# Performance work log

Hardware: AMD Instinct MI355X
Metric: run time of the kernel (lower is better)

The kernel has to match this reference:

```python
import jax, jax.numpy as jnp
import numpy as np

E, H, G, NB, T_OBS, A, PRED = 64, 128, 8, 32.0, 8, 512, 12


def setup_inputs() -> dict:
    key = jax.random.key(0)
    ks = jax.random.split(key, 12)
    s = lambda fan: 1.0 / np.sqrt(fan)
    obs = jax.random.uniform(ks[0], (T_OBS, A, 2), dtype=jnp.float32, minval=-40.0, maxval=40.0)
    mask = jax.random.uniform(ks[1], (A,)) > 0.1
    W_e = jax.random.normal(ks[2], (E, 2), jnp.float32) * s(2)
    b_e = jnp.zeros((E,), jnp.float32)
    W_p = jax.random.normal(ks[3], (H, G * G * H), jnp.float32) * s(G * G * H)
    b_p = jnp.zeros((H,), jnp.float32)
    W_ih = jax.random.normal(ks[4], (4 * H, E + H), jnp.float32) * s(E + H)
    W_hh = jax.random.normal(ks[5], (4 * H, H), jnp.float32) * s(H)
    b_ih = jnp.zeros((4 * H,), jnp.float32)
    b_hh = jnp.zeros((4 * H,), jnp.float32)
    W_o = jax.random.normal(ks[6], (5, H), jnp.float32) * s(H)
    b_o = jnp.zeros((5,), jnp.float32)
    return dict(obs=obs, mask=mask, W_e=W_e, b_e=b_e, W_p=W_p, b_p=b_p,
                W_ih=W_ih, W_hh=W_hh, b_ih=b_ih, b_hh=b_hh, W_o=W_o, b_o=b_o)


def _social_pool(hidden, pos, mask, W_p, b_p):
    # hidden (A,H), pos (A,2), mask (A,) -> pooled (A,H)
    a, h = hidden.shape
    cell = 2.0 * NB / G
    vi = mask & jnp.all(~jnp.isnan(pos), axis=-1)           # valid agents
    rel = pos[None, :, :] - pos[:, None, :]                  # rel[i,j] = pos[j]-pos[i]
    rx, ry = rel[..., 0], rel[..., 1]
    inb = (jnp.abs(rx) < NB) & (jnp.abs(ry) < NB)
    col = jnp.clip(jnp.floor((rx + NB) / cell).astype(jnp.int32), 0, G - 1)
    row = jnp.clip(jnp.floor((ry + NB) / cell).astype(jnp.int32), 0, G - 1)
    cell_id = row * G + col                                  # (A,A)
    eye = jnp.eye(a, dtype=bool)
    valid = vi[:, None] & vi[None, :] & (~eye) & inb
    onehot = jax.nn.one_hot(cell_id, G * G, dtype=hidden.dtype) * valid[..., None].astype(hidden.dtype)
    grid = jnp.einsum('ijg,jh->igh', onehot, hidden)         # (A, G*G, H) scatter-sum
    pooled = grid.reshape(a, G * G * h) @ W_p.T + b_p
    return jnp.where(vi[:, None], pooled, 0.0)


def _lstm(inp, h, c, W_ih, W_hh, b_ih, b_hh):
    z = inp @ W_ih.T + h @ W_hh.T + b_ih + b_hh
    i, f, g, o = jnp.split(z, 4, axis=-1)
    i, f, o = jax.nn.sigmoid(i), jax.nn.sigmoid(f), jax.nn.sigmoid(o)
    g = jnp.tanh(g)
    c = f * c + i * g
    return o * jnp.tanh(c), c


def _forward(obs, mask, W_e, b_e, W_p, b_p, W_ih, W_hh, b_ih, b_hh, W_o, b_o):
    a = obs.shape[1]
    obs_clean = jnp.where(jnp.isnan(obs), 0.0, obs)
    h0 = jnp.zeros((a, H), obs.dtype)
    c0 = jnp.zeros((a, H), obs.dtype)

    def enc_step(carry, pos):
        h, c = carry
        emb = jax.nn.relu(pos @ W_e.T + b_e)
        soc = _social_pool(h, pos, mask, W_p, b_p)
        h, c = _lstm(jnp.concatenate([emb, soc], -1), h, c, W_ih, W_hh, b_ih, b_hh)
        return (h, c), None

    (h, c), _ = jax.lax.scan(enc_step, (h0, c0), obs_clean)

    cur0 = jnp.where(mask[:, None], obs_clean[-1], 0.0)

    def dec_step(carry, _):
        h, c, cur = carry
        emb = jax.nn.relu(cur @ W_e.T + b_e)
        soc = _social_pool(h, cur, mask, W_p, b_p)
        h, c = _lstm(jnp.concatenate([emb, soc], -1), h, c, W_ih, W_hh, b_ih, b_hh)
        raw = h @ W_o.T + b_o                                # (A,5)
        mu = raw[:, :2]
        sg = jnp.exp(raw[:, 2:4]) + 1e-6
        rh = jnp.tanh(raw[:, 4])
        cur = cur + mu * mask[:, None].astype(raw.dtype)
        return (h, c, cur), (cur, sg, rh)

    _, (pred_mu, pred_sigma, pred_rho) = jax.lax.scan(dec_step, (h, c, cur0), None, length=PRED)
    return pred_mu, pred_sigma, pred_rho


def reference(obs, mask, W_e, b_e, W_p, b_p, W_ih, W_hh, b_ih, b_hh, W_o, b_o):
    return _forward(obs, mask, W_e, b_e, W_p, b_p, W_ih, W_hh, b_ih, b_hh, W_o, b_o)
```

## Files before the change

kernel.cpp:

```cpp
#include <hip/hip_runtime.h>

#define T_OBS 8
#define PRED  12

typedef __attribute__((ext_vector_type(8))) short bf16x8;
typedef __attribute__((ext_vector_type(4))) float f32x4;
typedef __attribute__((ext_vector_type(2))) unsigned long long u64x2;
#define MFMA16(a,b,c) __builtin_amdgcn_mfma_f32_16x16x32_bf16((a),(b),(c),0,0,0)

#define WP_OFF    0
#define WZ_OFF    2097152
#define BZ_OFF    2424832
#define MASK_OFF  2426880
#define CUR_OFF   2428928
#define HG_OFF    2433024
#define CST_OFF   2564096
#define XIN_OFF   2826240
#define U_OFF     3022848
#define LSTP_OFF  11411456
#define NVP_OFF   16130048

static __device__ __forceinline__ unsigned short f2bf(float x){
    union { float f; unsigned u; } v; v.f = x;
    unsigned r = v.u + 0x7fffu + ((v.u >> 16) & 1u);
    return (unsigned short)(r >> 16);
}
static __device__ __forceinline__ unsigned pack2(float a, float b){
    return (unsigned)f2bf(a) | ((unsigned)f2bf(b) << 16);
}
static __device__ __forceinline__ float bf2lo(unsigned v){ return __uint_as_float(v << 16); }
static __device__ __forceinline__ float bf2hi(unsigned v){ return __uint_as_float(v & 0xffff0000u); }
static __device__ __forceinline__ float sigm_f(float x){ return 1.f / (1.f + __expf(-x)); }
static __device__ __forceinline__ float tanh_f(float x){
    float e = __expf(-2.f * fabsf(x));
    float t = (1.f - e) / (1.f + e);
    return copysignf(t, x);
}

__global__ __launch_bounds__(256) void prep(
    const float* __restrict__ obs, const float* __restrict__ Wp,
    const float* __restrict__ Wih, const float* __restrict__ Whh,
    const float* __restrict__ bih, const float* __restrict__ bhh,
    const unsigned char* __restrict__ mraw,
    unsigned short* __restrict__ wp_bf, unsigned short* __restrict__ wz,
    float* __restrict__ bz, int* __restrict__ mski,
    unsigned* __restrict__ hg32, float* __restrict__ cst,
    short* __restrict__ lst_pre, int* __restrict__ nv_pre)
{
    __shared__ int maskl[512];
    __shared__ float2 posl[512];
    __shared__ short  celll[512];
    __shared__ int mflagA, mflagB;
    const int bid = blockIdx.x, tid = threadIdx.x;
    const int i0 = bid * 256 + tid, stride = 512 * 256;

    if (tid == 0){ mflagA = 0; mflagB = 0; }
    __syncthreads();
    for (int j = tid; j < 512; j += 256){
        unsigned char b = mraw[j];
        if (b && (j & 3))        atomicAdd(&mflagA, 1);
        if (b && ((j & 7) == 4)) atomicAdd(&mflagB, 1);
    }
    __syncthreads();
    for (int j = tid; j < 512; j += 256){
        int v;
        if (mflagA)      v = mraw[j] ? 1 : 0;
        else if (mflagB) v = ((const int*)mraw)[j] ? 1 : 0;
        else             v = ((const long long*)mraw)[j] ? 1 : 0;
        maskl[j] = v;
        if (bid == 0) mski[j] = v;
    }
    __syncthreads();

    for (int i = i0; i < 524288; i += stride)
        ((unsigned*)wp_bf)[i] = pack2(Wp[2*i], Wp[2*i + 1]);
    for (int i = i0; i < 81920; i += stride){
        int n = (2*i) / 320, k = (2*i) - n*320;
        float w0 = (k < 192)     ? Wih[n*192 + k]     : Whh[n*128 + k - 192];
        float w1 = (k + 1 < 192) ? Wih[n*192 + k + 1] : Whh[n*128 + k + 1 - 192];
        ((unsigned*)wz)[i] = pack2(w0, w1);
    }
    for (int i = i0; i < 512; i += stride) bz[i] = bih[i] + bhh[i];
    for (int i = i0; i < 32768; i += stride) hg32[i] = 0u;
    for (int i = i0; i < 65536; i += stride) cst[i] = 0.f;

    const int vi = maskl[bid];
    for (int tt = 0; tt <= 8; ++tt){
        const int to = (tt < 8) ? tt : 7;
        __syncthreads();
        for (int j = tid; j < 512; j += 256){
            float px = obs[to*1024 + 2*j], py = obs[to*1024 + 2*j + 1];
            if (isnan(px)) px = 0.f;
            if (isnan(py)) py = 0.f;
            if (tt == 8 && !maskl[j]){ px = 0.f; py = 0.f; }
            posl[j] = make_float2(px, py);
        }
        __syncthreads();
        const float2 pi = posl[bid];
        for (int j = tid; j < 512; j += 256){
            int cc = -1;
            if (vi && j != bid && maskl[j]){
                float rx = posl[j].x - pi.x, ry = posl[j].y - pi.y;
                if (fabsf(rx) < 32.f && fabsf(ry) < 32.f){
                    int col = (int)floorf((rx + 32.f) * 0.125f);
                    int row = (int)floorf((ry + 32.f) * 0.125f);
                    col = min(max(col, 0), 7); row = min(max(row, 0), 7);
                    cc = row*8 + col;
                }
            }
            celll[j] = (short)cc;
        }
        __syncthreads();
        if (tid < 64){
            short* lp = lst_pre + ((long long)tt*512 + bid)*512;
            int base = 0;
            for (int b = 0; b < 8; ++b){
                short cj = celll[b*64 + tid];
                bool val = cj >= 0;
                unsigned long long bal = __ballot(val);
                int pre = __popcll(bal & ((1ull << tid) - 1ull));
                if (val) lp[base + pre] = (short)((b*64 + tid) | ((int)cj << 9));
                base += __popcll(bal);
            }
            if (tid == 0) nv_pre[tt*512 + bid] = base;
        }
    }
}

__global__ __launch_bounds__(256) void ku(
    const unsigned short* __restrict__ hg,
    const unsigned short* __restrict__ wp_bf,
    const float* __restrict__ obs, const float* __restrict__ W_o,
    const float* __restrict__ b_o, const int* __restrict__ mski,
    float* __restrict__ cur, float* __restrict__ out,
    unsigned short* __restrict__ U, int t)
{
    __shared__ unsigned short ustage[32][256];
    const int bid = blockIdx.x, tid = threadIdx.x;

    if (t > T_OBS && tid < 64){
        const int dec_t = t - T_OBS - 1;
        unsigned v = ((const unsigned*)hg)[bid*64 + tid];
        float h0 = bf2lo(v), h1 = bf2hi(v);
        float p[5];
        #pragma unroll
        for (int o = 0; o < 5; ++o)
            p[o] = W_o[o*128 + 2*tid]*h0 + W_o[o*128 + 2*tid + 1]*h1;
        #pragma unroll
        for (int s = 32; s; s >>= 1)
            #pragma unroll
            for (int o = 0; o < 5; ++o) p[o] += __shfl_xor(p[o], s, 64);
        if (tid == 0){
            float mu0 = p[0] + b_o[0], mu1 = p[1] + b_o[1];
            float s0 = __expf(p[2] + b_o[2]) + 1e-6f;
            float s1 = __expf(p[3] + b_o[3]) + 1e-6f;
            float rh = tanh_f(p[4] + b_o[4]);
            float cx, cy;
            if (dec_t == 0){
                cx = obs[7*1024 + bid*2]; cy = obs[7*1024 + bid*2 + 1];
                if (isnan(cx)) cx = 0.f;
                if (isnan(cy)) cy = 0.f;
                if (!mski[bid]){ cx = 0.f; cy = 0.f; }
            } else {
                cx = cur[bid*2]; cy = cur[bid*2 + 1];
            }
            if (mski[bid]){ cx += mu0; cy += mu1; }
            cur[bid*2] = cx; cur[bid*2 + 1] = cy;
            out[dec_t*1024 + bid*2]             = cx;
            out[dec_t*1024 + bid*2 + 1]         = cy;
            out[12288 + dec_t*1024 + bid*2]     = s0;
            out[12288 + dec_t*1024 + bid*2 + 1] = s1;
            out[24576 + dec_t*512 + bid]        = rh;
        }
    }
    if (t >= T_OBS + PRED) return;

    const int mq = bid >> 5, cp = bid & 31;
    const int r0 = mq * 32;
    const int w = tid >> 6, lane = tid & 63;
    const int msub = w & 1, nq = w >> 1;
    const int lrow = lane & 15, lk = (lane >> 4) * 8;
    f32x4 acc[2][4] = {};
    #pragma unroll
    for (int ks = 0; ks < 4; ++ks){
        bf16x8 a = *(const bf16x8*)(hg + (r0 + msub*16 + lrow)*128 + ks*32 + lk);
        #pragma unroll
        for (int cell = 0; cell < 2; ++cell){
            #pragma unroll
            for (int ntl = 0; ntl < 4; ++ntl){
                const unsigned short* bp = wp_bf +
                    ((nq*4 + ntl)*16 + lrow)*8192 + (2*cp + cell)*128 + ks*32 + lk;
                acc[cell][ntl] = MFMA16(a, *(const bf16x8*)bp, acc[cell][ntl]);
            }
        }
    }
    const int crow = (lane >> 4) * 4, ccol = lane & 15;
    #pragma unroll
    for (int cell = 0; cell < 2; ++cell)
        #pragma unroll
        for (int ntl = 0; ntl < 4; ++ntl)
            #pragma unroll
            for (int r = 0; r < 4; ++r)
                ustage[msub*16 + crow + r][cell*128 + (nq*4 + ntl)*16 + ccol]
                    = f2bf(acc[cell][ntl][r]);
    __syncthreads();
    for (int e = tid; e < 1024; e += 256){
        int r = e >> 5, o = e & 31;
        u64x2 v = *(const u64x2*)&ustage[r][o*8];
        __builtin_nontemporal_store(v,
            (u64x2*)((char*)U + ((long long)(r0 + r)*64 + 2*cp)*256 + o*16));
    }
}

__global__ __launch_bounds__(256) void kg(
    const float* __restrict__ obs, const int* __restrict__ mski,
    const unsigned short* __restrict__ U,
    const float* __restrict__ W_e, const float* __restrict__ b_e,
    const float* __restrict__ b_p, const float* __restrict__ cur,
    const short* __restrict__ lst_pre, const int* __restrict__ nv_pre,
    unsigned short* __restrict__ xin, int t)
{
    __shared__ float2 pos[512];
    __shared__ short  cells_s[512];
    __shared__ short  lst[512];
    __shared__ int    nvS;
    __shared__ float  socp[8][128];
    const int bid = blockIdx.x, tid = threadIdx.x;

    float2 pi;
    int n;
    const int vi = mski[bid];

    if (t <= 8){
        const int to = (t < 8) ? t : 7;
        float px = obs[to*1024 + 2*bid], py = obs[to*1024 + 2*bid + 1];
        if (isnan(px)) px = 0.f;
        if (isnan(py)) py = 0.f;
        if (t == 8 && !vi){ px = 0.f; py = 0.f; }
        pi = make_float2(px, py);
        const short* lp = lst_pre + ((long long)t*512 + bid)*512;
        for (int e = tid; e < 512; e += 256) lst[e] = lp[e];
        n = (t == 0) ? 0 : nv_pre[t*512 + bid];
        __syncthreads();
    } else {
        for (int s = 0; s < 2; ++s){
            int j = tid + s*256;
            pos[j] = ((const float2*)cur)[j];
        }
        __syncthreads();
        pi = pos[bid];
        for (int s = 0; s < 2; ++s){
            int j = tid + s*256;
            int cc = -1;
            if (vi && j != bid && mski[j]){
                float rx = pos[j].x - pi.x, ry = pos[j].y - pi.y;
                if (fabsf(rx) < 32.f && fabsf(ry) < 32.f){
                    int col = (int)floorf((rx + 32.f) * 0.125f);
                    int row = (int)floorf((ry + 32.f) * 0.125f);
                    col = min(max(col, 0), 7); row = min(max(row, 0), 7);
                    cc = row*8 + col;
                }
            }
            cells_s[j] = (short)cc;
        }
        __syncthreads();
        if (tid < 64){
            int base = 0;
            for (int b = 0; b < 8; ++b){
                short cj = cells_s[b*64 + tid];
                bool val = cj >= 0;
                unsigned long long bal = __ballot(val);
                int pre = __popcll(bal & ((1ull << tid) - 1ull));
                if (val) lst[base + pre] = (short)((b*64 + tid) | ((int)cj << 9));
                base += __popcll(bal);
            }
            if (tid == 0) nvS = base;
        }
        __syncthreads();
        n = nvS;
    }

    {
        const int slot = tid >> 5, lq = tid & 31;
        const unsigned long long* ub = (const unsigned long long*)U;
        float s0 = 0.f, s1 = 0.f, s2 = 0.f, s3 = 0.f;
        int b4 = 0;
        for (; b4 + 128 <= n; b4 += 128){
            unsigned long long v[16];
            #pragma unroll
            for (int u = 0; u < 16; ++u){
                int pk = lst[b4 + u*8 + slot];
                v[u] = __builtin_nontemporal_load(
                           ub + (pk & 511)*2048 + (pk >> 9)*32 + lq);
            }
            #pragma unroll
            for (int u = 0; u < 16; ++u){
                unsigned lo = (unsigned)v[u], hi = (unsigned)(v[u] >> 32);
                s0 += bf2lo(lo); s1 += bf2hi(lo);
                s2 += bf2lo(hi); s3 += bf2hi(hi);
            }
        }
        for (; b4 + 32 <= n; b4 += 32){
            unsigned long long v[4];
            #pragma unroll
            for (int u = 0; u < 4; ++u){
                int pk = lst[b4 + u*8 + slot];
                v[u] = __builtin_nontemporal_load(
                           ub + (pk & 511)*2048 + (pk >> 9)*32 + lq);
            }
            #pragma unroll
            for (int u = 0; u < 4; ++u){
                unsigned lo = (unsigned)v[u], hi = (unsigned)(v[u] >> 32);
                s0 += bf2lo(lo); s1 += bf2hi(lo);
                s2 += bf2lo(hi); s3 += bf2hi(hi);
            }
        }
        for (; b4 + 8 <= n; b4 += 8){
            int pk = lst[b4 + slot];
            unsigned long long v = __builtin_nontemporal_load(
                                       ub + (pk & 511)*2048 + (pk >> 9)*32 + lq);
            unsigned lo = (unsigned)v, hi = (unsigned)(v >> 32);
            s0 += bf2lo(lo); s1 += bf2hi(lo); s2 += bf2lo(hi); s3 += bf2hi(hi);
        }
        if (b4 + slot < n){
            int pk = lst[b4 + slot];
            unsigned long long v = __builtin_nontemporal_load(
                                       ub + (pk & 511)*2048 + (pk >> 9)*32 + lq);
            unsigned lo = (unsigned)v, hi = (unsigned)(v >> 32);
            s0 += bf2lo(lo); s1 += bf2hi(lo); s2 += bf2lo(hi); s3 += bf2hi(hi);
        }
        f32x4 sv = {s0, s1, s2, s3};
        *(f32x4*)&socp[slot][lq*4] = sv;
    }
    __syncthreads();
    if (tid < 128){
        float s = b_p[tid];
        #pragma unroll
        for (int p = 0; p < 8; ++p) s += socp[p][tid];
        if (!vi) s = 0.f;
        xin[bid*192 + 64 + tid] = f2bf(s);
    } else if (tid < 192){
        int u = tid - 128;
        float e = W_e[u*2]*pi.x + W_e[u*2 + 1]*pi.y + b_e[u];
        xin[bid*192 + u] = f2bf(fmaxf(e, 0.f));
    }
}

__global__ __launch_bounds__(256) void kl(
    const unsigned short* __restrict__ xin, const unsigned short* __restrict__ hg_rd,
    const unsigned short* __restrict__ wz, const float* __restrict__ bz,
    float* __restrict__ cst, unsigned* __restrict__ hg_wr)
{
    __shared__ float zpart[2][4][16][16];
    __shared__ float hst[16][17];
    const int bid = blockIdx.x, tid = threadIdx.x;
    const int rt = bid >> 3, uo = bid & 7;
    const int r0 = rt * 16, u0 = uo * 16;
    const int w = tid >> 6, lane = tid & 63;
    const int gh = w & 1, p = w >> 1;
    const int lrow = lane & 15, lk = (lane >> 4) * 8;

    f32x4 acc[2] = {};
    #pragma unroll
    for (int kk = 0; kk < 5; ++kk){
        const int ks = p*5 + kk;
        const int row = r0 + lrow;
        bf16x8 a;
        if (ks < 6) a = *(const bf16x8*)(xin + row*192 + ks*32 + lk);
        else        a = *(const bf16x8*)(hg_rd + row*128 + (ks - 6)*32 + lk);
        #pragma unroll
        for (int gi = 0; gi < 2; ++gi){
            const int g = gh*2 + gi;
            bf16x8 b = *(const bf16x8*)(wz + (g*128 + u0 + lrow)*320 + ks*32 + lk);
            acc[gi] = MFMA16(a, b, acc[gi]);
        }
    }
    const int crow = (lane >> 4) * 4, ccol = lane & 15;
    #pragma unroll
    for (int gi = 0; gi < 2; ++gi)
        #pragma unroll
        for (int r = 0; r < 4; ++r)
            zpart[p][gh*2 + gi][crow + r][ccol] = acc[gi][r];
    __syncthreads();

    if (tid < 256){
        int row = tid >> 4, lu = tid & 15;
        int unit = u0 + lu;
        float zi = zpart[0][0][row][lu] + zpart[1][0][row][lu] + bz[      unit];
        float zf = zpart[0][1][row][lu] + zpart[1][1][row][lu] + bz[128 + unit];
        float zg = zpart[0][2][row][lu] + zpart[1][2][row][lu] + bz[256 + unit];
        float zo = zpart[0][3][row][lu] + zpart[1][3][row][lu] + bz[384 + unit];
        float ig = sigm_f(zi), fg = sigm_f(zf);
        float gv = tanh_f(zg), og = sigm_f(zo);
        int gi2 = (r0 + row)*128 + unit;
        float cn = fg * cst[gi2] + ig * gv;
        float hn = og * tanh_f(cn);
        cst[gi2] = cn;
        hst[row][lu] = hn;
    }
    __syncthreads();
    if (tid < 128){
        int row = tid >> 3, pp = tid & 7;
        hg_wr[(r0 + row)*64 + uo*8 + pp] = pack2(hst[row][2*pp], hst[row][2*pp + 1]);
    }
}

extern "C" void kernel_launch(void* const* d_in, const int* in_sizes, int n_in,
                              void* d_out, int out_size, void* d_ws, size_t ws_size,
                              hipStream_t stream)
{
    const float* obs  = (const float*)d_in[0];
    const unsigned char* mraw = (const unsigned char*)d_in[1];
    const float* W_e  = (const float*)d_in[2];
    const float* b_e  = (const float*)d_in[3];
    const float* W_p  = (const float*)d_in[4];
    const float* b_p  = (const float*)d_in[5];
    const float* W_ih = (const float*)d_in[6];
    const float* W_hh = (const float*)d_in[7];
    const float* b_ih = (const float*)d_in[8];
    const float* b_hh = (const float*)d_in[9];
    const float* W_o  = (const float*)d_in[10];
    const float* b_o  = (const float*)d_in[11];
    float* out = (float*)d_out;

    char* ws = (char*)d_ws;
    unsigned short* wp_bf = (unsigned short*)(ws + WP_OFF);
    unsigned short* wz_bf = (unsigned short*)(ws + WZ_OFF);
    float* bz   = (float*)(ws + BZ_OFF);
    int*   mski = (int*)  (ws + MASK_OFF);
    float* cur  = (float*)(ws + CUR_OFF);
    unsigned short* hg = (unsigned short*)(ws + HG_OFF);
    float* cst  = (float*)(ws + CST_OFF);
    unsigned short* xin = (unsigned short*)(ws + XIN_OFF);
    unsigned short* U   = (unsigned short*)(ws + U_OFF);
    short* lst_pre = (short*)(ws + LSTP_OFF);
    int*   nv_pre  = (int*)  (ws + NVP_OFF);

    prep<<<512, 256, 0, stream>>>(obs, W_p, W_ih, W_hh, b_ih, b_hh, mraw,
                                  wp_bf, wz_bf, bz, mski, (unsigned*)hg, cst,
                                  lst_pre, nv_pre);

    for (int t = 0; t < T_OBS + PRED; ++t){
        if (t > 0)
            ku<<<512, 256, 0, stream>>>(hg, wp_bf, obs, W_o, b_o, mski,
                                        cur, out, U, t);
        kg<<<512, 256, 0, stream>>>(obs, mski, U, W_e, b_e, b_p, cur,
                                    lst_pre, nv_pre, xin, t);
        kl<<<256, 256, 0, stream>>>(xin, hg, wz_bf, bz, cst, (unsigned*)hg);
    }
    ku<<<512, 256, 0, stream>>>(hg, wp_bf, obs, W_o, b_o, mski,
                                cur, out, U, T_OBS + PRED);
}
```

Before: 533.0 us.

## Fuse per-step pooling, LSTM and projection kernels with device-wide barriers

Replaces the three kernels launched per time step (ku, kg, kl) with a single step kernel. Inside it, a hand-rolled atomic grid barrier separates the gather, LSTM and projection/output phases, and the hidden state is double-buffered so reads and writes do not conflict across steps. This cuts about 60 launches and their gaps down to 20, and moves the decoder output head after the projection within the same step. In exchange it depends on all 512 blocks being co-resident (launch bounds of 2 blocks per CU) for the spin barrier to work. The spin loop has a bailout cap and uses relaxed atomics, which could cause hangs or incorrect results if that assumption fails.

Result: slower. 824.2 us (+54.6%).

```diff
diff --git a/kernel.cpp b/kernel.cpp
--- a/kernel.cpp
+++ b/kernel.cpp
@@ -2,23 +2,42 @@
 
 #define T_OBS 8
 #define PRED  12
+#define NSTEP 20
 
 typedef __attribute__((ext_vector_type(8))) short bf16x8;
 typedef __attribute__((ext_vector_type(4))) float f32x4;
 typedef __attribute__((ext_vector_type(2))) unsigned long long u64x2;
 #define MFMA16(a,b,c) __builtin_amdgcn_mfma_f32_16x16x32_bf16((a),(b),(c),0,0,0)
+#define AS __ATOMIC_RELAXED, __HIP_MEMORY_SCOPE_AGENT
 
 #define WP_OFF    0
 #define WZ_OFF    2097152
 #define BZ_OFF    2424832
 #define MASK_OFF  2426880
 #define CUR_OFF   2428928
-#define HG_OFF    2433024
-#define CST_OFF   2564096
-#define XIN_OFF   2826240
-#define U_OFF     3022848
-#define LSTP_OFF  11411456
-#define NVP_OFF   16130048
+#define HG0_OFF   2433024
+#define HG1_OFF   2564096
+#define CST_OFF   2695168
+#define XIN_OFF   2957312
+#define U_OFF     3153920
+#define LSTP_OFF  11542528
+#define NVP_OFF   16261120
+#define BAR_OFF   16279552
+
+static __device__ __forceinline__ void st32c(void* p, unsigned v){
+    __hip_atomic_store((unsigned*)p, v, AS);
+}
+static __device__ __forceinline__ unsigned ld32c(const void* p){
+    return __hip_atomic_load((const unsigned*)p, AS);
+}
+static __device__ __forceinline__ unsigned long long ld64c(const void* p){
+    return __hip_atomic_load((const unsigned long long*)p, AS);
+}
+static __device__ __forceinline__ bf16x8 ldfragc(const unsigned short* p){
+    union { unsigned long long q[2]; bf16x8 v; } u;
+    u.q[0] = ld64c(p); u.q[1] = ld64c(p + 4);
+    return u.v;
+}
 
 static __device__ __forceinline__ unsigned short f2bf(float x){
     union { float f; unsigned u; } v; v.f = x;
@@ -37,6 +56,25 @@
     return copysignf(t, x);
 }
 
+static __device__ __forceinline__ void gridbar(int* bar, int bid, int target){
+    __syncthreads();
+    if (threadIdx.x == 0){
+        int p = __hip_atomic_fetch_add(&bar[32 + (bid >> 3)*16], 1, AS);
+        if ((p & 7) == 7){
+            int q = __hip_atomic_fetch_add(&bar[16], 1, AS);
+            if ((q & 63) == 63)
+                __hip_atomic_store(&bar[0], target, AS);
+        }
+        int spins = 0;
+        while (__hip_atomic_load(&bar[0], AS) < target){
+            __builtin_amdgcn_s_sleep(1);
+            if (++spins > (1 << 22)) break;
+        }
+        asm volatile("" ::: "memory");
+    }
+    __syncthreads();
+}
+
 __global__ __launch_bounds__(256) void prep(
     const float* __restrict__ obs, const float* __restrict__ Wp,
     const float* __restrict__ Wih, const float* __restrict__ Whh,
@@ -44,8 +82,9 @@
     const unsigned char* __restrict__ mraw,
     unsigned short* __restrict__ wp_bf, unsigned short* __restrict__ wz,
     float* __restrict__ bz, int* __restrict__ mski,
-    unsigned* __restrict__ hg32, float* __restrict__ cst,
-    short* __restrict__ lst_pre, int* __restrict__ nv_pre)
+    unsigned* __restrict__ hg1, float* __restrict__ cst,
+    short* __restrict__ lst_pre, int* __restrict__ nv_pre,
+    int* __restrict__ bar)
 {
     __shared__ int maskl[512];
     __shared__ float2 posl[512];
@@ -81,8 +120,9 @@
         ((unsigned*)wz)[i] = pack2(w0, w1);
     }
     for (int i = i0; i < 512; i += stride) bz[i] = bih[i] + bhh[i];
-    for (int i = i0; i < 32768; i += stride) hg32[i] = 0u;
+    for (int i = i0; i < 32768; i += stride) hg1[i] = 0u;
     for (int i = i0; i < 65536; i += stride) cst[i] = 0.f;
+    for (int i = i0; i < 2048; i += stride) bar[i] = 0;
 
     const int vi = maskl[bid];
     for (int tt = 0; tt <= 8; ++tt){
@@ -127,281 +167,281 @@
     }
 }
 
-__global__ __launch_bounds__(256) void ku(
-    const unsigned short* __restrict__ hg,
-    const unsigned short* __restrict__ wp_bf,
-    const float* __restrict__ obs, const float* __restrict__ W_o,
-    const float* __restrict__ b_o, const int* __restrict__ mski,
-    float* __restrict__ cur, float* __restrict__ out,
-    unsigned short* __restrict__ U, int t)
+union StepSmem {
+    struct { float2 pos[512]; short cells[512]; short lst[512];
+             float socp[8][128]; } a;
+    struct { float zpart[2][4][16][16]; float hst[16][17]; } b;
+    struct { unsigned short ustage[32][256]; } c;
+};
+
+__global__ __launch_bounds__(256, 2) void step(
+    const float* __restrict__ obs, const int* __restrict__ mski,
+    const unsigned short* __restrict__ wp, const unsigned short* __restrict__ wz,
+    const float* __restrict__ bz, const float* __restrict__ b_p,
+    const float* __restrict__ W_e, const float* __restrict__ b_e,
+    const float* __restrict__ W_o, const float* __restrict__ b_o,
+    const short* __restrict__ lst_pre, const int* __restrict__ nv_pre,
+    float* __restrict__ cur, const unsigned short* __restrict__ hg_rd,
+    unsigned short* __restrict__ hg_wr, float* __restrict__ cst,
+    unsigned short* __restrict__ xin, unsigned short* __restrict__ U,
+    int* __restrict__ bar, float* __restrict__ out, int t)
 {
-    __shared__ unsigned short ustage[32][256];
+    __shared__ StepSmem sm;
+    __shared__ int nvS;
     const int bid = blockIdx.x, tid = threadIdx.x;
-
-    if (t > T_OBS && tid < 64){
-        const int dec_t = t - T_OBS - 1;
-        unsigned v = ((const unsigned*)hg)[bid*64 + tid];
-        float h0 = bf2lo(v), h1 = bf2hi(v);
-        float p[5];
+    const int w = tid >> 6, lane = tid & 63;
+    const int lrow = lane & 15, lk = (lane >> 4) * 8;
+    const int crow = (lane >> 4) * 4, ccol = lane & 15;
+
+    {
+        float2 pi;
+        int n;
+        const int vi = mski[bid];
+        if (t <= 8){
+            const int to = (t < 8) ? t : 7;
+            float px = obs[to*1024 + 2*bid], py = obs[to*1024 + 2*bid + 1];
+            if (isnan(px)) px = 0.f;
+            if (isnan(py)) py = 0.f;
+            if (t == 8 && !vi){ px = 0.f; py = 0.f; }
+            pi = make_float2(px, py);
+            const short* lp = lst_pre + ((long long)t*512 + bid)*512;
+            for (int e = tid; e < 512; e += 256) sm.a.lst[e] = lp[e];
+            n = (t == 0) ? 0 : nv_pre[t*512 + bid];
+            __syncthreads();
+        } else {
+            for (int s = 0; s < 2; ++s){
+                int j = tid + s*256;
+                sm.a.pos[j] = ((const float2*)cur)[j];
+            }
+            __syncthreads();
+            pi = sm.a.pos[bid];
+            for (int s = 0; s < 2; ++s){
+                int j = tid + s*256;
+                int cc = -1;
+                if (vi && j != bid && mski[j]){
+                    float rx = sm.a.pos[j].x - pi.x, ry = sm.a.pos[j].y - pi.y;
+                    if (fabsf(rx) < 32.f && fabsf(ry) < 32.f){
+                        int col = (int)floorf((rx + 32.f) * 0.125f);
+                        int row = (int)floorf((ry + 32.f) * 0.125f);
+                        col = min(max(col, 0), 7); row = min(max(row, 0), 7);
+                        cc = row*8 + col;
+                    }
+                }
+                sm.a.cells[j] = (short)cc;
+            }
+            __syncthreads();
+            if (tid < 64){
+                int base = 0;
+                for (int b = 0; b < 8; ++b){
+                    short cj = sm.a.cells[b*64 + tid];
+                    bool val = cj >= 0;
+                    unsigned long long bal = __ballot(val);
+                    int pre = __popcll(bal & ((1ull << tid) - 1ull));
+                    if (val) sm.a.lst[base + pre] = (short)((b*64 + tid) | ((int)cj << 9));
+                    base += __popcll(bal);
+                }
+                if (tid == 0) nvS = base;
+            }
+            __syncthreads();
+            n = nvS;
+        }
+        {
+            const int slot = tid >> 5, lq = tid & 31;
+            const unsigned long long* ub = (const unsigned long long*)U;
+            float s0 = 0.f, s1 = 0.f, s2 = 0.f, s3 = 0.f;
+            int b4 = 0;
+            for (; b4 + 128 <= n; b4 += 128){
+                unsigned long long v[16];
+                #pragma unroll
+                for (int u = 0; u < 16; ++u){
+                    int pk = sm.a.lst[b4 + u*8 + slot];
+                    v[u] = __builtin_nontemporal_load(
+                               ub + (pk & 511)*2048 + (pk >> 9)*32 + lq);
+                }
+                #pragma unroll
+                for (int u = 0; u < 16; ++u){
+                    unsigned lo = (unsigned)v[u], hi = (unsigned)(v[u] >> 32);
+                    s0 += bf2lo(lo); s1 += bf2hi(lo);
+                    s2 += bf2lo(hi); s3 += bf2hi(hi);
+                }
+            }
+            for (; b4 + 32 <= n; b4 += 32){
+                unsigned long long v[4];
+                #pragma unroll
+                for (int u = 0; u < 4; ++u){
+                    int pk = sm.a.lst[b4 + u*8 + slot];
+                    v[u] = __builtin_nontemporal_load(
+                               ub + (pk & 511)*2048 + (pk >> 9)*32 + lq);
+                }
+                #pragma unroll
+                for (int u = 0; u < 4; ++u){
+                    unsigned lo = (unsigned)v[u], hi = (unsigned)(v[u] >> 32);
+                    s0 += bf2lo(lo); s1 += bf2hi(lo);
+                    s2 += bf2lo(hi); s3 += bf2hi(hi);
+                }
+            }
+            for (; b4 + 8 <= n; b4 += 8){
+                int pk = sm.a.lst[b4 + slot];
+                unsigned long long v = __builtin_nontemporal_load(
+                                           ub + (pk & 511)*2048 + (pk >> 9)*32 + lq);
+                unsigned lo = (unsigned)v, hi = (unsigned)(v >> 32);
+                s0 += bf2lo(lo); s1 += bf2hi(lo); s2 += bf2lo(hi); s3 += bf2hi(hi);
+            }
+            if (b4 + slot < n){
+                int pk = sm.a.lst[b4 + slot];
+                unsigned long long v = __builtin_nontemporal_load(
+                                           ub + (pk & 511)*2048 + (pk >> 9)*32 + lq);
+                unsigned lo = (unsigned)v, hi = (unsigned)(v >> 32);
+                s0 += bf2lo(lo); s1 += bf2hi(lo); s2 += bf2lo(hi); s3 += bf2hi(hi);
+            }
+            f32x4 sv = {s0, s1, s2, s3};
+            *(f32x4*)&sm.a.socp[slot][lq*4] = sv;
+        }
+        __syncthreads();
+        unsigned* xin32 = (unsigned*)xin;
+        if (tid < 64){
+            float s0 = b_p[2*tid], s1 = b_p[2*tid + 1];
+            #pragma unroll
+            for (int p = 0; p < 8; ++p){
+                s0 += sm.a.socp[p][2*tid];
+                s1 += sm.a.socp[p][2*tid + 1];
+            }
+            if (!vi){ s0 = 0.f; s1 = 0.f; }
+            st32c(xin32 + bid*96 + 32 + tid, pack2(s0, s1));
+        } else if (tid < 96){
+            int u = tid - 64;
+            float e0 = fmaxf(W_e[(2*u    )*2]*pi.x + W_e[(2*u    )*2 + 1]*pi.y + b_e[2*u    ], 0.f);
+            float e1 = fmaxf(W_e[(2*u + 1)*2]*pi.x + W_e[(2*u + 1)*2 + 1]*pi.y + b_e[2*u + 1], 0.f);
+            st32c(xin32 + bid*96 + u, pack2(e0, e1));
+        }
+    }
+    gridbar(bar, bid, 2*t + 1);
+
+    if (bid < 256){
+        const int rt = bid >> 3, uo = bid & 7;
+        const int r0 = rt * 16, u0 = uo * 16;
+        const int gh = w & 1, p = w >> 1;
+
+        f32x4 acc[2] = {};
         #pragma unroll
-        for (int o = 0; o < 5; ++o)
-            p[o] = W_o[o*128 + 2*tid]*h0 + W_o[o*128 + 2*tid + 1]*h1;
+        for (int kk = 0; kk < 5; ++kk){
+            const int ks = p*5 + kk;
+            const int row = r0 + lrow;
+            bf16x8 a;
+            if (ks < 6) a = ldfragc(xin + row*192 + ks*32 + lk);
+            else        a = *(const bf16x8*)(hg_rd + row*128 + (ks - 6)*32 + lk);
+            #pragma unroll
+            for (int gi = 0; gi < 2; ++gi){
+                const int g = gh*2 + gi;
+                bf16x8 b = *(const bf16x8*)(wz + (g*128 + u0 + lrow)*320 + ks*32 + lk);
+                acc[gi] = MFMA16(a, b, acc[gi]);
+            }
+        }
         #pragma unroll
-        for (int s = 32; s; s >>= 1)
-            #pragma unroll
-            for (int o = 0; o < 5; ++o) p[o] += __shfl_xor(p[o], s, 64);
-        if (tid == 0){
-            float mu0 = p[0] + b_o[0], mu1 = p[1] + b_o[1];
-            float s0 = __expf(p[2] + b_o[2]) + 1e-6f;
-            float s1 = __expf(p[3] + b_o[3]) + 1e-6f;
-            float rh = tanh_f(p[4] + b_o[4]);
-            float cx, cy;
-            if (dec_t == 0){
-                cx = obs[7*1024 + bid*2]; cy = obs[7*1024 + bid*2 + 1];
-                if (isnan(cx)) cx = 0.f;
-                if (isnan(cy)) cy = 0.f;
-                if (!mski[bid]){ cx = 0.f; cy = 0.f; }
-            } else {
-                cx = cur[bid*2]; cy = cur[bid*2 + 1];
-            }
-            if (mski[bid]){ cx += mu0; cy += mu1; }
-            cur[bid*2] = cx; cur[bid*2 + 1] = cy;
-            out[dec_t*1024 + bid*2]             = cx;
-            out[dec_t*1024 + bid*2 + 1]         = cy;
-            out[12288 + dec_t*1024 + bid*2]     = s0;
-            out[12288 + dec_t*1024 + bid*2 + 1] = s1;
-            out[24576 + dec_t*512 + bid]        = rh;
-        }
-    }
-    if (t >= T_OBS + PRED) return;
+        for (int gi = 0; gi < 2; ++gi)
+            #pragma unroll
+            for (int r = 0; r < 4; ++r)
+                sm.b.zpart[p][gh*2 + gi][crow + r][ccol] = acc[gi][r];
+        __syncthreads();
+
+        {
+            int row = tid >> 4, lu = tid & 15;
+            int unit = u0 + lu;
+            float zi = sm.b.zpart[0][0][row][lu] + sm.b.zpart[1][0][row][lu] + bz[      unit];
+            float zf = sm.b.zpart[0][1][row][lu] + sm.b.zpart[1][1][row][lu] + bz[128 + unit];
+            float zg = sm.b.zpart[0][2][row][lu] + sm.b.zpart[1][2][row][lu] + bz[256 + unit];
+            float zo = sm.b.zpart[0][3][row][lu] + sm.b.zpart[1][3][row][lu] + bz[384 + unit];
+            float ig = sigm_f(zi), fg = sigm_f(zf);
+            float gv = tanh_f(zg), og = sigm_f(zo);
+            int gi2 = (r0 + row)*128 + unit;
+            float cn = fg * cst[gi2] + ig * gv;
+            float hn = og * tanh_f(cn);
+            cst[gi2] = cn;
+            sm.b.hst[row][lu] = hn;
+        }
+        __syncthreads();
+        if (tid < 128){
+            int row = tid >> 3, pp = tid & 7;
+            st32c((unsigned*)hg_wr + (r0 + row)*64 + uo*8 + pp,
+                  pack2(sm.b.hst[row][2*pp], sm.b.hst[row][2*pp + 1]));
+        }
+    }
+    gridbar(bar, bid, 2*t + 2);
 
     const int mq = bid >> 5, cp = bid & 31;
-    const int r0 = mq * 32;
-    const int w = tid >> 6, lane = tid & 63;
-    const int msub = w & 1, nq = w >> 1;
-    const int lrow = lane & 15, lk = (lane >> 4) * 8;
-    f32x4 acc[2][4] = {};
-    #pragma unroll
-    for (int ks = 0; ks < 4; ++ks){
-        bf16x8 a = *(const bf16x8*)(hg + (r0 + msub*16 + lrow)*128 + ks*32 + lk);
+    const int r0c = mq * 32;
+    if (t < NSTEP - 1){
+        const int msub = w & 1, nq = w >> 1;
+        bf16x8 afr[4];
         #pragma unroll
-        for (int cell = 0; cell < 2; ++cell){
-            #pragma unroll
-            for (int ntl = 0; ntl < 4; ++ntl){
-                const unsigned short* bp = wp_bf +
-                    ((nq*4 + ntl)*16 + lrow)*8192 + (2*cp + cell)*128 + ks*32 + lk;
-                acc[cell][ntl] = MFMA16(a, *(const bf16x8*)bp, acc[cell][ntl]);
-            }
-        }
-    }
-    const int crow = (lane >> 4) * 4, ccol = lane & 15;
-    #pragma unroll
-    for (int cell = 0; cell < 2; ++cell)
+        for (int ks = 0; ks < 4; ++ks)
+            afr[ks] = ldfragc(hg_wr + (r0c + msub*16 + lrow)*128 + ks*32 + lk);
+        f32x4 acc[2][4] = {};
         #pragma unroll
-        for (int ntl = 0; ntl < 4; ++ntl)
-            #pragma unroll
-            for (int r = 0; r < 4; ++r)
-                ustage[msub*16 + crow + r][cell*128 + (nq*4 + ntl)*16 + ccol]
-                    = f2bf(acc[cell][ntl][r]);
-    __syncthreads();
-    for (int e = tid; e < 1024; e += 256){
-        int r = e >> 5, o = e & 31;
-        u64x2 v = *(const u64x2*)&ustage[r][o*8];
-        __builtin_nontemporal_store(v,
-            (u64x2*)((char*)U + ((long long)(r0 + r)*64 + 2*cp)*256 + o*16));
-    }
-}
-
-__global__ __launch_bounds__(256) void kg(
-    const float* __restrict__ obs, const int* __restrict__ mski,
-    const unsigned short* __restrict__ U,
-    const float* __restrict__ W_e, const float* __restrict__ b_e,
-    const float* __restrict__ b_p, const float* __restrict__ cur,
-    const short* __restrict__ lst_pre, const int* __restrict__ nv_pre,
-    unsigned short* __restrict__ xin, int t)
-{
-    __shared__ float2 pos[512];
-    __shared__ short  cells_s[512];
-    __shared__ short  lst[512];
-    __shared__ int    nvS;
-    __shared__ float  socp[8][128];
-    const int bid = blockIdx.x, tid = threadIdx.x;
-
-    float2 pi;
-    int n;
-    const int vi = mski[bid];
-
-    if (t <= 8){
-        const int to = (t < 8) ? t : 7;
-        float px = obs[to*1024 + 2*bid], py = obs[to*1024 + 2*bid + 1];
-        if (isnan(px)) px = 0.f;
-        if (isnan(py)) py = 0.f;
-        if (t == 8 && !vi){ px = 0.f; py = 0.f; }
-        pi = make_float2(px, py);
-        const short* lp = lst_pre + ((long long)t*512 + bid)*512;
-        for (int e = tid; e < 512; e += 256) lst[e] = lp[e];
-        n = (t == 0) ? 0 : nv_pre[t*512 + bid];
-        __syncthreads();
-    } else {
-        for (int s = 0; s < 2; ++s){
-            int j = tid + s*256;
-            pos[j] = ((const float2*)cur)[j];
-        }
-        __syncthreads();
-        pi = pos[bid];
-        for (int s = 0; s < 2; ++s){
-            int j = tid + s*256;
-            int cc = -1;
-            if (vi && j != bid && mski[j]){
-                float rx = pos[j].x - pi.x, ry = pos[j].y - pi.y;
-                if (fabsf(rx) < 32.f && fabsf(ry) < 32.f){
-                    int col = (int)floorf((rx + 32.f) * 0.125f);
-                    int row = (int)floorf((ry + 32.f) * 0.125f);
-                    col = min(max(col, 0), 7); row = min(max(row, 0), 7);
-                    cc = row*8 + col;
-                }
-            }
-            cells_s[j] = (short)cc;
-        }
-        __syncthreads();
-        if (tid < 64){
-            int base = 0;
-            for (int b = 0; b < 8; ++b){
-                short cj = cells_s[b*64 + tid];
-                bool val = cj >= 0;
-                unsigned long long bal = __ballot(val);
-                int pre = __popcll(bal & ((1ull << tid) - 1ull));
-                if (val) lst[base + pre] = (short)((b*64 + tid) | ((int)cj << 9));
-                base += __popcll(bal);
-            }
-            if (tid == 0) nvS = base;
-        }
-        __syncthreads();
-        n = nvS;
-    }
-
-    {
-        const int slot = tid >> 5, lq = tid & 31;
-        const unsigned long long* ub = (const unsigned long long*)U;
-        float s0 = 0.f, s1 = 0.f, s2 = 0.f, s3 = 0.f;
-        int b4 = 0;
-        for (; b4 + 128 <= n; b4 += 128){
-            unsigned long long v[16];
-            #pragma unroll
-            for (int u = 0; u < 16; ++u){
-                int pk = lst[b4 + u*8 + slot];
-                v[u] = __builtin_nontemporal_load(
-                           ub + (pk & 511)*2048 + (pk >> 9)*32 + lq);
-            }
-            #pragma unroll
-            for (int u = 0; u < 16; ++u){
-                unsigned lo = (unsigned)v[u], hi = (unsigned)(v[u] >> 32);
-                s0 += bf2lo(lo); s1 += bf2hi(lo);
-                s2 += bf2lo(hi); s3 += bf2hi(hi);
-            }
-        }
-        for (; b4 + 32 <= n; b4 += 32){
-            unsigned long long v[4];
-            #pragma unroll
-            for (int u = 0; u < 4; ++u){
-                int pk = lst[b4 + u*8 + slot];
-                v[u] = __builtin_nontemporal_load(
-                           ub + (pk & 511)*2048 + (pk >> 9)*32 + lq);
-            }
-            #pragma unroll
-            for (int u = 0; u < 4; ++u){
-                unsigned lo = (unsigned)v[u], hi = (unsigned)(v[u] >> 32);
-                s0 += bf2lo(lo); s1 += bf2hi(lo);
-                s2 += bf2lo(hi); s3 += bf2hi(hi);
-            }
-        }
-        for (; b4 + 8 <= n; b4 += 8){
-            int pk = lst[b4 + slot];
-            unsigned long long v = __builtin_nontemporal_load(
-                                       ub + (pk & 511)*2048 + (pk >> 9)*32 + lq);
-            unsigned lo = (unsigned)v, hi = (unsigned)(v >> 32);
-            s0 += bf2lo(lo); s1 += bf2hi(lo); s2 += bf2lo(hi); s3 += bf2hi(hi);
-        }
-        if (b4 + slot < n){
-            int pk = lst[b4 + slot];
-            unsigned long long v = __builtin_nontemporal_load(
-                                       ub + (pk & 511)*2048 + (pk >> 9)*32 + lq);
-            unsigned lo = (unsigned)v, hi = (unsigned)(v >> 32);
-            s0 += bf2lo(lo); s1 += bf2hi(lo); s2 += bf2lo(hi); s3 += bf2hi(hi);
-        }
-        f32x4 sv = {s0, s1, s2, s3};
-        *(f32x4*)&socp[slot][lq*4] = sv;
-    }
-    __syncthreads();
-    if (tid < 128){
-        float s = b_p[tid];
+        for (int ks = 0; ks < 4; ++ks){
+            #pragma unroll
+            for (int cell = 0; cell < 2; ++cell){
+                #pragma unroll
+                for (int ntl = 0; ntl < 4; ++ntl){
+                    const unsigned short* bp = wp +
+                        ((nq*4 + ntl)*16 + lrow)*8192 + (2*cp + cell)*128 + ks*32 + lk;
+                    acc[cell][ntl] = MFMA16(afr[ks], *(const bf16x8*)bp, acc[cell][ntl]);
+                }
+            }
+        }
         #pragma unroll
-        for (int p = 0; p < 8; ++p) s += socp[p][tid];
-        if (!vi) s = 0.f;
-        xin[bid*192 + 64 + tid] = f2bf(s);
-    } else if (tid < 192){
-        int u = tid - 128;
-        float e = W_e[u*2]*pi.x + W_e[u*2 + 1]*pi.y + b_e[u];
-        xin[bid*192 + u] = f2bf(fmaxf(e, 0.f));
-    }
-}
-
-__global__ __launch_bounds__(256) void kl(
-    const unsigned short* __restrict__ xin, const unsigned short* __restrict__ hg_rd,
-    const unsigned short* __restrict__ wz, const float* __restrict__ bz,
-    float* __restrict__ cst, unsigned* __restrict__ hg_wr)
-{
-    __shared__ float zpart[2][4][16][16];
-    __shared__ float hst[16][17];
-    const int bid = blockIdx.x, tid = threadIdx.x;
-    const int rt = bid >> 3, uo = bid & 7;
-    const int r0 = rt * 16, u0 = uo * 16;
-    const int w = tid >> 6, lane = tid & 63;
-    const int gh = w & 1, p = w >> 1;
-    const int lrow = lane & 15, lk = (lane >> 4) * 8;
-
-    f32x4 acc[2] = {};
-    #pragma unroll
-    for (int kk = 0; kk < 5; ++kk){
-        const int ks = p*5 + kk;
-        const int row = r0 + lrow;
-        bf16x8 a;
-        if (ks < 6) a = *(const bf16x8*)(xin + row*192 + ks*32 + lk);
-        else        a = *(const bf16x8*)(hg_rd + row*128 + (ks - 6)*32 + lk);
-        #pragma unroll
-        for (int gi = 0; gi < 2; ++gi){
-            const int g = gh*2 + gi;
-            bf16x8 b = *(const bf16x8*)(wz + (g*128 + u0 + lrow)*320 + ks*32 + lk);
-            acc[gi] = MFMA16(a, b, acc[gi]);
-        }
-    }
-    const int crow = (lane >> 4) * 4, ccol = lane & 15;
-    #pragma unroll
-    for (int gi = 0; gi < 2; ++gi)
-        #pragma unroll
-        for (int r = 0; r < 4; ++r)
-            zpart[p][gh*2 + gi][crow + r][ccol] = acc[gi][r];
-    __syncthreads();
-
-    if (tid < 256){
-        int row = tid >> 4, lu = tid & 15;
-        int unit = u0 + lu;
-        float zi = zpart[0][0][row][lu] + zpart[1][0][row][lu] + bz[      unit];
-        float zf = zpart[0][1][row][lu] + zpart[1][1][row][lu] + bz[128 + unit];
-        float zg = zpart[0][2][row][lu] + zpart[1][2][row][lu] + bz[256 + unit];
-        float zo = zpart[0][3][row][lu] + zpart[1][3][row][lu] + bz[384 + unit];
-        float ig = sigm_f(zi), fg = sigm_f(zf);
-        float gv = tanh_f(zg), og = sigm_f(zo);
-        int gi2 = (r0 + row)*128 + unit;
-        float cn = fg * cst[gi2] + ig * gv;
-        float hn = og * tanh_f(cn);
-        cst[gi2] = cn;
-        hst[row][lu] = hn;
-    }
-    __syncthreads();
-    if (tid < 128){
-        int row = tid >> 3, pp = tid & 7;
-        hg_wr[(r0 + row)*64 + uo*8 + pp] = pack2(hst[row][2*pp], hst[row][2*pp + 1]);
+        for (int cell = 0; cell < 2; ++cell)
+            #pragma unroll
+            for (int ntl = 0; ntl < 4; ++ntl)
+                #pragma unroll
+                for (int r = 0; r < 4; ++r)
+                    sm.c.ustage[msub*16 + crow + r][cell*128 + (nq*4 + ntl)*16 + ccol]
+                        = f2bf(acc[cell][ntl][r]);
+        __syncthreads();
+        for (int e = tid; e < 1024; e += 256){
+            int r = e >> 5, o = e & 31;
+            u64x2 v = *(const u64x2*)&sm.c.ustage[r][o*8];
+            __builtin_nontemporal_store(v,
+                (u64x2*)((char*)U + ((long long)(r0c + r)*64 + 2*cp)*256 + o*16));
+        }
+    }
+    if (t >= T_OBS && cp == 0){
+        const int dec_t = t - T_OBS;
+        for (int s = 0; s < 8; ++s){
+            int ag = r0c + w*8 + s;
+            unsigned hv = ld32c((const unsigned*)hg_wr + ag*64 + lane);
+            float h0 = bf2lo(hv), h1 = bf2hi(hv);
+            float pr[5];
+            #pragma unroll
+            for (int o = 0; o < 5; ++o)
+                pr[o] = W_o[o*128 + 2*lane]*h0 + W_o[o*128 + 2*lane + 1]*h1;
+            #pragma unroll
+            for (int sh = 32; sh; sh >>= 1)
+                #pragma unroll
+                for (int o = 0; o < 5; ++o) pr[o] += __shfl_xor(pr[o], sh, 64);
+            if (lane == 0){
+                float mu0 = pr[0] + b_o[0], mu1 = pr[1] + b_o[1];
+                float s0 = __expf(pr[2] + b_o[2]) + 1e-6f;
+                float s1 = __expf(pr[3] + b_o[3]) + 1e-6f;
+                float rh = tanh_f(pr[4] + b_o[4]);
+                float cx, cy;
+                if (dec_t == 0){
+                    cx = obs[7*1024 + ag*2]; cy = obs[7*1024 + ag*2 + 1];
+                    if (isnan(cx)) cx = 0.f;
+                    if (isnan(cy)) cy = 0.f;
+                    if (!mski[ag]){ cx = 0.f; cy = 0.f; }
+                } else {
+                    cx = cur[ag*2]; cy = cur[ag*2 + 1];
+                }
+                if (mski[ag]){ cx += mu0; cy += mu1; }
+                cur[ag*2] = cx; cur[ag*2 + 1] = cy;
+                out[dec_t*1024 + ag*2]             = cx;
+                out[dec_t*1024 + ag*2 + 1]         = cy;
+                out[12288 + dec_t*1024 + ag*2]     = s0;
+                out[12288 + dec_t*1024 + ag*2 + 1] = s1;
+                out[24576 + dec_t*512 + ag]        = rh;
+            }
+        }
     }
 }
 
@@ -429,25 +469,23 @@
     float* bz   = (float*)(ws + BZ_OFF);
     int*   mski = (int*)  (ws + MASK_OFF);
     float* cur  = (float*)(ws + CUR_OFF);
-    unsigned short* hg = (unsigned short*)(ws + HG_OFF);
+    unsigned short* hg[2] = { (unsigned short*)(ws + HG0_OFF),
+                              (unsigned short*)(ws + HG1_OFF) };
     float* cst  = (float*)(ws + CST_OFF);
     unsigned short* xin = (unsigned short*)(ws + XIN_OFF);
     unsigned short* U   = (unsigned short*)(ws + U_OFF);
     short* lst_pre = (short*)(ws + LSTP_OFF);
     int*   nv_pre  = (int*)  (ws + NVP_OFF);
+    int*   bar     = (int*)  (ws + BAR_OFF);
 
     prep<<<512, 256, 0, stream>>>(obs, W_p, W_ih, W_hh, b_ih, b_hh, mraw,
-                                  wp_bf, wz_bf, bz, mski, (unsigned*)hg, cst,
-                                  lst_pre, nv_pre);
-
-    for (int t = 0; t < T_OBS + PRED; ++t){
-        if (t > 0)
-            ku<<<512, 256, 0, stream>>>(hg, wp_bf, obs, W_o, b_o, mski,
-                                        cur, out, U, t);
-        kg<<<512, 256, 0, stream>>>(obs, mski, U, W_e, b_e, b_p, cur,
-                                    lst_pre, nv_pre, xin, t);
-        kl<<<256, 256, 0, stream>>>(xin, hg, wz_bf, bz, cst, (unsigned*)hg);
-    }
-    ku<<<512, 256, 0, stream>>>(hg, wp_bf, obs, W_o, b_o, mski,
-                                cur, out, U, T_OBS + PRED);
-}
+                                  wp_bf, wz_bf, bz, mski,
+                                  (unsigned*)hg[1], cst, lst_pre, nv_pre, bar);
+
+    for (int t = 0; t < NSTEP; ++t){
+        step<<<512, 256, 0, stream>>>(obs, mski, wp_bf, wz_bf, bz, b_p,
+                                      W_e, b_e, W_o, b_o, lst_pre, nv_pre,
+                                      cur, hg[(t + 1) & 1], hg[t & 1],
+                                      cst, xin, U, bar, out, t);
+    }
+}
```
